# Kernel tuning notes

Hardware: AMD Instinct MI355X
Metric: run time of the kernel (lower is better)

The kernel has to match this reference:

```python
import jax, jax.numpy as jnp
import numpy as np

EMBED_DIM = 768
NUM_HEADS = 12
HEAD_DIM = EMBED_DIM // NUM_HEADS


def setup_inputs() -> dict:
    key = jax.random.key(0)
    k1, k2, k3, k4, k5 = jax.random.split(key, 5)
    x_q = jax.random.normal(k1, (8, 1024, EMBED_DIM), dtype=jnp.float32)
    s = 1.0 / np.sqrt(EMBED_DIM)
    qkv_w = jax.random.uniform(k2, (3 * EMBED_DIM, EMBED_DIM), jnp.float32, -s, s)
    qkv_b = jax.random.uniform(k3, (3 * EMBED_DIM,), jnp.float32, -s, s)
    out_w = jax.random.uniform(k4, (EMBED_DIM, EMBED_DIM), jnp.float32, -s, s)
    out_b = jax.random.uniform(k5, (EMBED_DIM,), jnp.float32, -s, s)
    return {"x_q": x_q, "qkv_w": qkv_w, "qkv_b": qkv_b, "out_w": out_w, "out_b": out_b}


def reference(x_q, qkv_w, qkv_b, out_w, out_b):
    b, p, c = x_q.shape
    scaling = HEAD_DIM ** (-0.5)
    # qkv projection: [b, p, 3c]
    qkv = x_q @ qkv_w.T + qkv_b
    qkv = qkv.reshape(b, p, 3, NUM_HEADS, HEAD_DIM)
    q = qkv[:, :, 0].transpose(0, 2, 1, 3) * scaling  # [b, h, p, d]
    k = qkv[:, :, 1].transpose(0, 2, 1, 3)
    v = qkv[:, :, 2].transpose(0, 2, 1, 3)
    attn = jnp.einsum('bhqd,bhkd->bhqk', q, k)
    attn = jax.nn.softmax(attn, axis=-1)
    out = jnp.einsum('bhqk,bhkd->bhqd', attn, v)
    out = out.transpose(0, 2, 1, 3).reshape(b, p, c)
    return out @ out_w.T + out_b
```

## Files before the change

### kernel.cpp

```cpp
#include <hip/hip_runtime.h>
#include <stdint.h>

typedef float  f32x4 __attribute__((ext_vector_type(4)));
typedef int    i32x4 __attribute__((ext_vector_type(4)));
typedef short  bf16x8 __attribute__((ext_vector_type(8)));
typedef unsigned short u16;
typedef unsigned int   u32;

#define DEVINL __device__ __forceinline__

DEVINL u16 f2bf(float f) {
  u32 u = __builtin_bit_cast(u32, f);
  u32 r = u + 0x7fffu + ((u >> 16) & 1u);
  return (u16)(r >> 16);
}

DEVINL u32 cvtpk(float lo, float hi) {
  u32 r;
  asm("v_cvt_pk_bf16_f32 %0, %1, %2" : "=v"(r) : "v"(lo), "v"(hi));
  return r;
}

DEVINL void mfma16(f32x4& d, i32x4 a, i32x4 b) {
  d = __builtin_amdgcn_mfma_f32_16x16x32_bf16(
      __builtin_bit_cast(bf16x8, a), __builtin_bit_cast(bf16x8, b), d, 0, 0, 0);
}

#define GLD16(gp, lp) __builtin_amdgcn_global_load_lds( \
    (__attribute__((address_space(1))) void*)(gp), \
    (__attribute__((address_space(3))) void*)(lp), 16, 0, 0)

__global__ void cvt3_f32_bf16(const float* __restrict__ s0, u16* __restrict__ d0, int n0,
                              const float* __restrict__ s1, u16* __restrict__ d1, int n1,
                              const float* __restrict__ s2, u16* __restrict__ d2, int n2) {
  int i = blockIdx.x * blockDim.x + threadIdx.x;
  int stride = gridDim.x * blockDim.x;
  int nt = n0 + n1 + n2;
  for (; i < nt; i += stride) {
    const float* s; u16* d; int j = i;
    if (j < n0) { s = s0; d = d0; }
    else if ((j -= n0) < n1) { s = s1; d = d1; }
    else { j -= n1; s = s2; d = d2; }
    float4 v = ((const float4*)s)[j];
    ushort4 o;
    o.x = f2bf(v.x); o.y = f2bf(v.y); o.z = f2bf(v.z); o.w = f2bf(v.w);
    ((ushort4*)d)[j] = o;
  }
}

template<int BM, int BN, int FM, int FN, int EPI>
__global__ __launch_bounds__(256) void gemm_bt(
    const u16* __restrict__ A, const u16* __restrict__ Bw,
    int M, int N, const float* __restrict__ bias,
    float* __restrict__ Cf, u16* __restrict__ Qb, u16* __restrict__ Kb, u16* __restrict__ Vtb)
{
  constexpr int BK = 32;
  constexpr int K  = 768;
  constexpr int ABYT = BM * BK * 2;
  constexpr int BBYT = BN * BK * 2;
  __shared__ __align__(16) unsigned char sm[2 * (ABYT + BBYT)];

  const int tid = threadIdx.x;
  const int l   = tid & 63;
  const int wid = tid >> 6;
  const int wm  = wid >> 1, wn = wid & 1;
  const int g4  = l >> 4;
  const int c15 = l & 15;

  const int ntiles = N / BN;
  const int wg  = ntiles * (M / BM);
  const int per = wg >> 3;
  const int tile = ((int)blockIdx.x & 7) * per + ((int)blockIdx.x >> 3);
  const int mbase = (tile / ntiles) * BM;
  const int nbase = (tile % ntiles) * BN;

  auto stage = [&](int buf, int kt) {
    unsigned char* ab = sm + buf * (ABYT + BBYT);
    unsigned char* bb = ab + ABYT;
    #pragma unroll
    for (int c = 0; c < BM / 64; ++c) {
      int ch = c * 256 + tid;
      int row = ch & (BM - 1), pl = ch / BM;
      GLD16(A + (size_t)(mbase + row) * K + kt * BK + pl * 8, ab + ch * 16);
    }
    #pragma unroll
    for (int c = 0; c < BN / 64; ++c) {
      int ch = c * 256 + tid;
      int row = ch & (BN - 1), pl = ch / BN;
      GLD16(Bw + (size_t)(nbase + row) * K + kt * BK + pl * 8, bb + ch * 16);
    }
  };

  f32x4 acc[FM][FN] = {};

  stage(0, 0);
  __syncthreads();

  for (int kt = 0; kt < K / BK; ++kt) {
    int cur = kt & 1;
    if (kt + 1 < K / BK) stage(cur ^ 1, kt + 1);
    unsigned char* ab = sm + cur * (ABYT + BBYT);
    unsigned char* bb = ab + ABYT;
    i32x4 af[FM], bf[FN];
    #pragma unroll
    for (int mt = 0; mt < FM; ++mt) {
      int row = wm * (BM / 2) + mt * 16 + c15;
      af[mt] = *(const i32x4*)(ab + (g4 * BM + row) * 16);
    }
    #pragma unroll
    for (int nt = 0; nt < FN; ++nt) {
      int row = wn * (BN / 2) + nt * 16 + c15;
      bf[nt] = *(const i32x4*)(bb + (g4 * BN + row) * 16);
    }
    __builtin_amdgcn_s_setprio(1);
    #pragma unroll
    for (int mt = 0; mt < FM; ++mt)
      #pragma unroll
      for (int nt = 0; nt < FN; ++nt)
        mfma16(acc[mt][nt], af[mt], bf[nt]);
    __builtin_amdgcn_s_setprio(0);
    __syncthreads();
  }

  if constexpr (EPI == 0) {
    #pragma unroll
    for (int nt = 0; nt < FN; ++nt) {
      int n = nbase + wn * (BN / 2) + nt * 16 + c15;
      float bv = bias[n];
      #pragma unroll
      for (int mt = 0; mt < FM; ++mt) {
        int m0 = mbase + wm * (BM / 2) + mt * 16 + g4 * 4;
        float* dst = Cf + (size_t)m0 * N + n;
        #pragma unroll
        for (int j = 0; j < 4; ++j) dst[(size_t)j * N] = acc[mt][nt][j] + bv;
      }
    }
  } else {
    #pragma unroll
    for (int nt = 0; nt < FN; ++nt) {
      int n = nbase + wn * (BN / 2) + nt * 16 + c15;
      int which = n / 768;
      int rem = n - which * 768;
      int h = rem >> 6, d = rem & 63;
      float bv = bias[n];
      #pragma unroll
      for (int mt = 0; mt < FM; ++mt) {
        int m0 = mbase + wm * (BM / 2) + mt * 16 + g4 * 4;
        int b = m0 >> 10, p0 = m0 & 1023;
        int bh = b * 12 + h;
        if (which == 0) {
          u16* dst = Qb + ((size_t)bh * 1024 + p0) * 64 + d;
          #pragma unroll
          for (int j = 0; j < 4; ++j) dst[(size_t)j * 64] = f2bf((acc[mt][nt][j] + bv) * 0.125f);
        } else if (which == 1) {
          u16* dst = Kb + ((size_t)bh * 1024 + p0) * 64 + d;
          #pragma unroll
          for (int j = 0; j < 4; ++j) dst[(size_t)j * 64] = f2bf(acc[mt][nt][j] + bv);
        } else {
          uint2 uu;
          uu.x = cvtpk(acc[mt][nt][0] + bv, acc[mt][nt][1] + bv);
          uu.y = cvtpk(acc[mt][nt][2] + bv, acc[mt][nt][3] + bv);
          *(uint2*)(Vtb + ((size_t)bh * 64 + d) * 1024 + p0) = uu;
        }
      }
    }
  }
}

__global__ __launch_bounds__(256) void attn_fwd(
    const u16* __restrict__ Qb, const u16* __restrict__ Kb,
    const u16* __restrict__ Vtb, u16* __restrict__ Ob)
{
  __shared__ __align__(16) unsigned char sm[16384 + 4 * 8192];
  const int tid = threadIdx.x;
  const int l = tid & 63, wid = tid >> 6;
  const int g4 = l >> 4, c15 = l & 15;
  const int bid = blockIdx.x;
  const int bh = bid % 96, qt = bid / 96;

  const size_t bhoff = (size_t)bh * (1024 * 64);
  const u16* Qg = Qb + bhoff + (size_t)qt * 128 * 64;
  const u16* Kg = Kb + bhoff;
  const u16* Vg = Vtb + bhoff;

  #pragma unroll
  for (int c = 0; c < 4; ++c) {
    int ch = c * 256 + tid;
    int row = ch & 127, pl = ch >> 7;
    GLD16(Qg + (size_t)row * 64 + pl * 8, sm + ch * 16);
  }

  auto stageKV = [&](int buf, int t) {
    unsigned char* kb_ = sm + 16384 + buf * 8192;
    unsigned char* vb_ = sm + 32768 + buf * 8192;
    #pragma unroll
    for (int c = 0; c < 2; ++c) {
      int ch = c * 256 + tid;
      int row = ch & 63, pl = ch >> 6;
      GLD16(Kg + (size_t)(t * 64 + row) * 64 + pl * 8, kb_ + ch * 16);
      GLD16(Vg + (size_t)row * 1024 + t * 64 + pl * 8, vb_ + ch * 16);
    }
  };

  stageKV(0, 0);
  __syncthreads();

  i32x4 qf[2][2];
  #pragma unroll
  for (int qn = 0; qn < 2; ++qn)
    #pragma unroll
    for (int ks = 0; ks < 2; ++ks) {
      int row = wid * 32 + qn * 16 + c15;
      qf[qn][ks] = *(const i32x4*)(sm + ((ks * 4 + g4) * 128 + row) * 16);
    }
  __syncthreads();

  unsigned char* pw = sm + wid * 4096;

  const i32x4 ones = {0x3F803F80, 0x3F803F80, 0x3F803F80, 0x3F803F80};
  constexpr float LOG2E = 1.44269504f;

  f32x4 ot[4][2] = {};
  f32x4 lacc[2] = {};
  float mrow[2] = {-1e30f, -1e30f};
  float mc[2]   = {-1e30f, -1e30f};

  for (int t = 0; t < 16; ++t) {
    int cur = t & 1;
    if (t + 1 < 16) stageKV(cur ^ 1, t + 1);
    unsigned char* kb_ = sm + 16384 + cur * 8192;
    unsigned char* vb_ = sm + 32768 + cur * 8192;

    f32x4 st[4][2] = {};
    __builtin_amdgcn_s_setprio(1);
    #pragma unroll
    for (int ks = 0; ks < 2; ++ks)
      #pragma unroll
      for (int kmt = 0; kmt < 4; ++kmt) {
        i32x4 ka = *(const i32x4*)(kb_ + ((ks * 4 + g4) * 64 + kmt * 16 + c15) * 16);
        mfma16(st[kmt][0], ka, qf[0][ks]);
        mfma16(st[kmt][1], ka, qf[1][ks]);
      }
    __builtin_amdgcn_s_setprio(0);

    #pragma unroll
    for (int qn = 0; qn < 2; ++qn) {
      float mx = fmaxf(fmaxf(fmaxf(st[0][qn][0], st[0][qn][1]), fmaxf(st[0][qn][2], st[0][qn][3])),
                       fmaxf(fmaxf(st[1][qn][0], st[1][qn][1]), fmaxf(st[1][qn][2], st[1][qn][3])));
      mx = fmaxf(mx,
           fmaxf(fmaxf(fmaxf(st[2][qn][0], st[2][qn][1]), fmaxf(st[2][qn][2], st[2][qn][3])),
                 fmaxf(fmaxf(st[3][qn][0], st[3][qn][1]), fmaxf(st[3][qn][2], st[3][qn][3]))));
      mx = fmaxf(mx, __shfl_xor(mx, 16));
      mx = fmaxf(mx, __shfl_xor(mx, 32));
      if (!__all(mx - mrow[qn] <= 8.0f)) {
        float mnew = fmaxf(mrow[qn], mx);
        float sfq = exp2f((mrow[qn] - mnew) * LOG2E);
        mrow[qn] = mnew;
        mc[qn] = mnew * LOG2E;
        #pragma unroll
        for (int dmt = 0; dmt < 4; ++dmt)
          #pragma unroll
          for (int j = 0; j < 4; ++j) ot[dmt][qn][j] *= sfq;
        lacc[qn][0] *= sfq;
      }
      #pragma unroll
      for (int kmt = 0; kmt < 4; ++kmt) {
        float p0 = exp2f(__builtin_fmaf(st[kmt][qn][0], LOG2E, -mc[qn]));
        float p1 = exp2f(__builtin_fmaf(st[kmt][qn][1], LOG2E, -mc[qn]));
        float p2 = exp2f(__builtin_fmaf(st[kmt][qn][2], LOG2E, -mc[qn]));
        float p3 = exp2f(__builtin_fmaf(st[kmt][qn][3], LOG2E, -mc[qn]));
        int k0 = kmt * 16 + 4 * g4;
        uint2 ww;
        ww.x = cvtpk(p0, p1);
        ww.y = cvtpk(p2, p3);
        *(uint2*)(pw + ((k0 >> 3) * 32 + qn * 16 + c15) * 16 + (k0 & 7) * 2) = ww;
      }
    }

    i32x4 pb[2][2];
    #pragma unroll
    for (int qn = 0; qn < 2; ++qn)
      #pragma unroll
      for (int ks = 0; ks < 2; ++ks)
        pb[qn][ks] = *(const i32x4*)(pw + (((ks * 4 + g4) * 32) + qn * 16 + c15) * 16);

    __builtin_amdgcn_s_setprio(1);
    #pragma unroll
    for (int ks = 0; ks < 2; ++ks) {
      #pragma unroll
      for (int dmt = 0; dmt < 4; ++dmt) {
        i32x4 va = *(const i32x4*)(vb_ + ((ks * 4 + g4) * 64 + dmt * 16 + c15) * 16);
        mfma16(ot[dmt][0], va, pb[0][ks]);
        mfma16(ot[dmt][1], va, pb[1][ks]);
      }
      mfma16(lacc[0], ones, pb[0][ks]);
      mfma16(lacc[1], ones, pb[1][ks]);
    }
    __builtin_amdgcn_s_setprio(0);
    __syncthreads();
  }

  const int b = bh / 12, h = bh % 12;
  #pragma unroll
  for (int qn = 0; qn < 2; ++qn) {
    float inv = 1.0f / lacc[qn][0];
    int q = qt * 128 + wid * 32 + qn * 16 + c15;
    size_t rowoff = ((size_t)(b * 1024 + q) * 12 + h) * 64;
    #pragma unroll
    for (int dmt = 0; dmt < 4; ++dmt) {
      int d0 = dmt * 16 + g4 * 4;
      uint2 uu;
      uu.x = cvtpk(ot[dmt][qn][0] * inv, ot[dmt][qn][1] * inv);
      uu.y = cvtpk(ot[dmt][qn][2] * inv, ot[dmt][qn][3] * inv);
      *(uint2*)(Ob + rowoff + d0) = uu;
    }
  }
}

extern "C" void kernel_launch(void* const* d_in, const int* in_sizes, int n_in,
                              void* d_out, int out_size, void* d_ws, size_t ws_size,
                              hipStream_t stream) {
  const float* x    = (const float*)d_in[0];
  const float* qkvw = (const float*)d_in[1];
  const float* qkvb = (const float*)d_in[2];
  const float* outw = (const float*)d_in[3];
  const float* outb = (const float*)d_in[4];
  float* out = (float*)d_out;

  unsigned char* ws = (unsigned char*)d_ws;
  u16* xb  = (u16*)(ws);
  u16* wqb = (u16*)(ws + 12582912);
  u16* wob = (u16*)(ws + 16121856);
  u16* Qbf = (u16*)(ws + 17301504);
  u16* Kbf = (u16*)(ws + 29884416);
  u16* Vtb = (u16*)(ws + 42467328);
  u16* Ob  = xb;

  cvt3_f32_bf16<<<dim3(2048), dim3(256), 0, stream>>>(
      x, xb, 8192 * 768 / 4, qkvw, wqb, 2304 * 768 / 4, outw, wob, 768 * 768 / 4);

  gemm_bt<128, 128, 4, 4, 1><<<dim3(1152), dim3(256), 0, stream>>>(
      xb, wqb, 8192, 2304, qkvb, nullptr, Qbf, Kbf, Vtb);

  attn_fwd<<<dim3(768), dim3(256), 0, stream>>>(Qbf, Kbf, Vtb, Ob);

  gemm_bt<128, 64, 4, 2, 0><<<dim3(768), dim3(256), 0, stream>>>(
      Ob, wob, 8192, 768, outb, out, nullptr, nullptr, nullptr);
}
```

Measured before the change: 175.7 us.

## Double GEMM K-tile depth and read K/V directly from global in attention

New measurement: 245.0 us. 1.39x slower.

```diff
diff --git a/kernel.cpp b/kernel.cpp
--- a/kernel.cpp
+++ b/kernel.cpp
@@ -54,8 +54,9 @@
     int M, int N, const float* __restrict__ bias,
     float* __restrict__ Cf, u16* __restrict__ Qb, u16* __restrict__ Kb, u16* __restrict__ Vtb)
 {
-  constexpr int BK = 32;
+  constexpr int BK = 64;
   constexpr int K  = 768;
+  constexpr int T  = K / BK;
   constexpr int ABYT = BM * BK * 2;
   constexpr int BBYT = BN * BK * 2;
   __shared__ __align__(16) unsigned char sm[2 * (ABYT + BBYT)];
@@ -78,13 +79,13 @@
     unsigned char* ab = sm + buf * (ABYT + BBYT);
     unsigned char* bb = ab + ABYT;
     #pragma unroll
-    for (int c = 0; c < BM / 64; ++c) {
+    for (int c = 0; c < BM / 32; ++c) {
       int ch = c * 256 + tid;
       int row = ch & (BM - 1), pl = ch / BM;
       GLD16(A + (size_t)(mbase + row) * K + kt * BK + pl * 8, ab + ch * 16);
     }
     #pragma unroll
-    for (int c = 0; c < BN / 64; ++c) {
+    for (int c = 0; c < BN / 32; ++c) {
       int ch = c * 256 + tid;
       int row = ch & (BN - 1), pl = ch / BN;
       GLD16(Bw + (size_t)(nbase + row) * K + kt * BK + pl * 8, bb + ch * 16);
@@ -96,28 +97,34 @@
   stage(0, 0);
   __syncthreads();
 
-  for (int kt = 0; kt < K / BK; ++kt) {
+  for (int kt = 0; kt < T; ++kt) {
     int cur = kt & 1;
-    if (kt + 1 < K / BK) stage(cur ^ 1, kt + 1);
+    if (kt + 1 < T) stage(cur ^ 1, kt + 1);
     unsigned char* ab = sm + cur * (ABYT + BBYT);
     unsigned char* bb = ab + ABYT;
-    i32x4 af[FM], bf[FN];
-    #pragma unroll
-    for (int mt = 0; mt < FM; ++mt) {
-      int row = wm * (BM / 2) + mt * 16 + c15;
-      af[mt] = *(const i32x4*)(ab + (g4 * BM + row) * 16);
-    }
-    #pragma unroll
-    for (int nt = 0; nt < FN; ++nt) {
-      int row = wn * (BN / 2) + nt * 16 + c15;
-      bf[nt] = *(const i32x4*)(bb + (g4 * BN + row) * 16);
-    }
+    i32x4 af[FM][2], bf[FN][2];
+    #pragma unroll
+    for (int mt = 0; mt < FM; ++mt)
+      #pragma unroll
+      for (int ks = 0; ks < 2; ++ks) {
+        int row = wm * (BM / 2) + mt * 16 + c15;
+        af[mt][ks] = *(const i32x4*)(ab + ((ks * 4 + g4) * BM + row) * 16);
+      }
+    #pragma unroll
+    for (int nt = 0; nt < FN; ++nt)
+      #pragma unroll
+      for (int ks = 0; ks < 2; ++ks) {
+        int row = wn * (BN / 2) + nt * 16 + c15;
+        bf[nt][ks] = *(const i32x4*)(bb + ((ks * 4 + g4) * BN + row) * 16);
+      }
     __builtin_amdgcn_s_setprio(1);
     #pragma unroll
     for (int mt = 0; mt < FM; ++mt)
       #pragma unroll
       for (int nt = 0; nt < FN; ++nt)
-        mfma16(acc[mt][nt], af[mt], bf[nt]);
+        #pragma unroll
+        for (int ks = 0; ks < 2; ++ks)
+          mfma16(acc[mt][nt], af[mt][ks], bf[nt][ks]);
     __builtin_amdgcn_s_setprio(0);
     __syncthreads();
   }
@@ -151,11 +158,11 @@
         if (which == 0) {
           u16* dst = Qb + ((size_t)bh * 1024 + p0) * 64 + d;
           #pragma unroll
-          for (int j = 0; j < 4; ++j) dst[(size_t)j * 64] = f2bf((acc[mt][nt][j] + bv) * 0.125f);
+          for (int jj = 0; jj < 4; ++jj) dst[(size_t)jj * 64] = f2bf((acc[mt][nt][jj] + bv) * 0.125f);
         } else if (which == 1) {
           u16* dst = Kb + ((size_t)bh * 1024 + p0) * 64 + d;
           #pragma unroll
-          for (int j = 0; j < 4; ++j) dst[(size_t)j * 64] = f2bf(acc[mt][nt][j] + bv);
+          for (int jj = 0; jj < 4; ++jj) dst[(size_t)jj * 64] = f2bf(acc[mt][nt][jj] + bv);
         } else {
           uint2 uu;
           uu.x = cvtpk(acc[mt][nt][0] + bv, acc[mt][nt][1] + bv);
@@ -171,7 +178,7 @@
     const u16* __restrict__ Qb, const u16* __restrict__ Kb,
     const u16* __restrict__ Vtb, u16* __restrict__ Ob)
 {
-  __shared__ __align__(16) unsigned char sm[16384 + 4 * 8192];
+  __shared__ __align__(16) unsigned char sm[16384];
   const int tid = threadIdx.x;
   const int l = tid & 63, wid = tid >> 6;
   const int g4 = l >> 4, c15 = l & 15;
@@ -189,20 +196,6 @@
     int row = ch & 127, pl = ch >> 7;
     GLD16(Qg + (size_t)row * 64 + pl * 8, sm + ch * 16);
   }
-
-  auto stageKV = [&](int buf, int t) {
-    unsigned char* kb_ = sm + 16384 + buf * 8192;
-    unsigned char* vb_ = sm + 32768 + buf * 8192;
-    #pragma unroll
-    for (int c = 0; c < 2; ++c) {
-      int ch = c * 256 + tid;
-      int row = ch & 63, pl = ch >> 6;
-      GLD16(Kg + (size_t)(t * 64 + row) * 64 + pl * 8, kb_ + ch * 16);
-      GLD16(Vg + (size_t)row * 1024 + t * 64 + pl * 8, vb_ + ch * 16);
-    }
-  };
-
-  stageKV(0, 0);
   __syncthreads();
 
   i32x4 qf[2][2];
@@ -226,18 +219,13 @@
   float mc[2]   = {-1e30f, -1e30f};
 
   for (int t = 0; t < 16; ++t) {
-    int cur = t & 1;
-    if (t + 1 < 16) stageKV(cur ^ 1, t + 1);
-    unsigned char* kb_ = sm + 16384 + cur * 8192;
-    unsigned char* vb_ = sm + 32768 + cur * 8192;
-
     f32x4 st[4][2] = {};
     __builtin_amdgcn_s_setprio(1);
     #pragma unroll
     for (int ks = 0; ks < 2; ++ks)
       #pragma unroll
       for (int kmt = 0; kmt < 4; ++kmt) {
-        i32x4 ka = *(const i32x4*)(kb_ + ((ks * 4 + g4) * 64 + kmt * 16 + c15) * 16);
+        i32x4 ka = *(const i32x4*)(Kg + (size_t)(t * 64 + kmt * 16 + c15) * 64 + (ks * 4 + g4) * 8);
         mfma16(st[kmt][0], ka, qf[0][ks]);
         mfma16(st[kmt][1], ka, qf[1][ks]);
       }
@@ -289,7 +277,7 @@
     for (int ks = 0; ks < 2; ++ks) {
       #pragma unroll
       for (int dmt = 0; dmt < 4; ++dmt) {
-        i32x4 va = *(const i32x4*)(vb_ + ((ks * 4 + g4) * 64 + dmt * 16 + c15) * 16);
+        i32x4 va = *(const i32x4*)(Vg + (size_t)(dmt * 16 + c15) * 1024 + t * 64 + (ks * 4 + g4) * 8);
         mfma16(ot[dmt][0], va, pb[0][ks]);
         mfma16(ot[dmt][1], va, pb[1][ks]);
       }
@@ -297,7 +285,6 @@
       mfma16(lacc[1], ones, pb[1][ks]);
     }
     __builtin_amdgcn_s_setprio(0);
-    __syncthreads();
   }
 
   const int b = bh / 12, h = bh % 12;
```
